# Optimization experiments

Measured on AMD Instinct MI355X. Metric: run time of the kernel, lower is better.

The kernel has to match this reference:

```python
import jax, jax.numpy as jnp
import numpy as np

NUM_FEATURES = 5
HIDDEN = 64
NUM_CLASSES = 5
N_NODES = 100000
N_EDGES = 1600000


def setup_inputs() -> dict:
    key = jax.random.key(0)
    ks = jax.random.split(key, 8)
    x = jax.random.normal(ks[0], (N_NODES, 4, NUM_FEATURES), dtype=jnp.float32)
    edge_index = jax.random.randint(ks[1], (2, N_EDGES), 0, N_NODES, dtype=jnp.int64)
    batch = jnp.zeros((N_NODES,), dtype=jnp.int64)
    # GCNConv layer 1: 5 -> 64, layer 2: 64 -> 64, output Linear: 64 -> 5
    W1 = jax.random.normal(ks[2], (NUM_FEATURES, HIDDEN), dtype=jnp.float32) / np.sqrt(NUM_FEATURES)
    b1 = jnp.zeros((HIDDEN,), dtype=jnp.float32)
    W2 = jax.random.normal(ks[3], (HIDDEN, HIDDEN), dtype=jnp.float32) / np.sqrt(HIDDEN)
    b2 = jnp.zeros((HIDDEN,), dtype=jnp.float32)
    Wout = jax.random.normal(ks[4], (HIDDEN, NUM_CLASSES), dtype=jnp.float32) / np.sqrt(HIDDEN)
    bout = jnp.zeros((NUM_CLASSES,), dtype=jnp.float32)
    return {"x": x, "edge_index": edge_index, "batch": batch,
            "W1": W1, "b1": b1, "W2": W2, "b2": b2, "Wout": Wout, "bout": bout}


def reference(x, edge_index, batch, W1, b1, W2, b2, Wout, bout):
    N = x.shape[0]
    src, dst = edge_index[0], edge_index[1]
    # GCN symmetric normalization with self-loops: deg counts incoming edges + self loop
    deg = jax.ops.segment_sum(jnp.ones(src.shape, jnp.float32), dst, num_segments=N) + 1.0
    dinv_sqrt = jax.lax.rsqrt(deg)
    norm = dinv_sqrt[src] * dinv_sqrt[dst]            # [E]
    self_norm = (1.0 / deg)[:, None]                  # self-loop weight deg^-1

    def gcn_conv(h, W, b):
        h = h @ W                                     # [N, out]
        agg = jax.ops.segment_sum(h[src] * norm[:, None], dst, num_segments=N)
        return agg + h * self_norm + b

    h = jax.nn.relu(gcn_conv(x[:, -1, :], W1, b1))    # [N, HIDDEN]
    h = jax.nn.relu(gcn_conv(h, W2, b2))              # [N, HIDDEN]
    return jax.nn.softmax(h @ Wout + bout, axis=1)    # [N, 5]
```

## Files before the change

kernel.cpp:

```cpp
#include <hip/hip_runtime.h>
#include <hip/hip_fp16.h>

#define HID 64
#define NF 5
#define NC 5

#define WSH 9
#define WINN 512
#define NBMAX 256
#define SRCB 17
#define NBLK 512


__global__ __launch_bounds__(512) void k_bcount(const int* __restrict__ dst, int E, int chunk,
                                                int nb, int* __restrict__ cntmat) {
    __shared__ int cnt[NBMAX];
    int t = threadIdx.x;
    for (int i = t; i < nb; i += 512) cnt[i] = 0;
    __syncthreads();
    int c0 = blockIdx.x * chunk;
    int c1 = c0 + chunk; if (c1 > E) c1 = E;
    for (int i = c0 + t * 4; i < c1; i += 512 * 4) {
        if (i + 3 < c1) {
            int4 d4 = *reinterpret_cast<const int4*>(dst + i);
            atomicAdd(&cnt[d4.x >> WSH], 1);
            atomicAdd(&cnt[d4.y >> WSH], 1);
            atomicAdd(&cnt[d4.z >> WSH], 1);
            atomicAdd(&cnt[d4.w >> WSH], 1);
        } else {
            for (int k = i; k < c1; ++k) atomicAdd(&cnt[dst[k] >> WSH], 1);
        }
    }
    __syncthreads();
    for (int i = t; i < nb; i += 512) cntmat[blockIdx.x * nb + i] = cnt[i];
}

__global__ __launch_bounds__(NBLK) void k_wscan(int* __restrict__ cntmat, int nb,
                                                int* __restrict__ btot) {
    __shared__ int s[NBLK];
    int b = blockIdx.x;
    int t = threadIdx.x;
    int v = cntmat[t * nb + b];
    s[t] = v;
    __syncthreads();
    for (int o = 1; o < NBLK; o <<= 1) {
        int u = (t >= o) ? s[t - o] : 0;
        __syncthreads();
        s[t] += u;
        __syncthreads();
    }
    cntmat[t * nb + b] = s[t] - v;
    if (t == NBLK - 1) btot[b] = s[t];
}

__global__ __launch_bounds__(256) void k_bscan2(const int* __restrict__ btot, int nb, int N,
                                                int* __restrict__ bbase,
                                                int* __restrict__ offsets) {
    __shared__ int s[256];
    int t = threadIdx.x;
    int v = (t < nb) ? btot[t] : 0;
    s[t] = v;
    __syncthreads();
    for (int o = 1; o < 256; o <<= 1) {
        int u = (t >= o) ? s[t - o] : 0;
        __syncthreads();
        s[t] += u;
        __syncthreads();
    }
    if (t < nb) bbase[t] = s[t] - v;
    if (t == nb - 1) { bbase[nb] = s[t]; offsets[N] = s[t]; }
}

__global__ __launch_bounds__(512) void k_bfill(const int* __restrict__ src,
                                               const int* __restrict__ dst, int E, int chunk,
                                               int nb, const int* __restrict__ bbase,
                                               const int* __restrict__ cntmat,
                                               unsigned int* __restrict__ pairbuf) {
    __shared__ int wcur[NBMAX];
    int t = threadIdx.x;
    int blk = blockIdx.x;
    for (int i = t; i < nb; i += 512)
        wcur[i] = bbase[i] + cntmat[blk * nb + i];
    __syncthreads();
    int c0 = blk * chunk;
    int c1 = c0 + chunk; if (c1 > E) c1 = E;
    for (int i = c0 + t * 4; i < c1; i += 512 * 4) {
        if (i + 3 < c1) {
            int4 d4 = *reinterpret_cast<const int4*>(dst + i);
            int4 s4 = *reinterpret_cast<const int4*>(src + i);
            int p;
            p = atomicAdd(&wcur[d4.x >> WSH], 1);
            pairbuf[p] = ((unsigned)(d4.x & (WINN - 1)) << SRCB) | (unsigned)s4.x;
            p = atomicAdd(&wcur[d4.y >> WSH], 1);
            pairbuf[p] = ((unsigned)(d4.y & (WINN - 1)) << SRCB) | (unsigned)s4.y;
            p = atomicAdd(&wcur[d4.z >> WSH], 1);
            pairbuf[p] = ((unsigned)(d4.z & (WINN - 1)) << SRCB) | (unsigned)s4.z;
            p = atomicAdd(&wcur[d4.w >> WSH], 1);
            pairbuf[p] = ((unsigned)(d4.w & (WINN - 1)) << SRCB) | (unsigned)s4.w;
        } else {
            for (int k = i; k < c1; ++k) {
                int d = dst[k];
                int p = atomicAdd(&wcur[d >> WSH], 1);
                pairbuf[p] = ((unsigned)(d & (WINN - 1)) << SRCB) | (unsigned)src[k];
            }
        }
    }
}

__global__ __launch_bounds__(WINN) void k_csr(const unsigned int* __restrict__ pairbuf,
                                              const int* __restrict__ bbase, int N,
                                              const float* __restrict__ x,
                                              int* __restrict__ offsets,
                                              int* __restrict__ csr_src,
                                              float* __restrict__ dinv,
                                              float* __restrict__ xs8) {
    int b = blockIdx.x, t = threadIdx.x;
    int lane = t & 63, w = t >> 6;
    int winStart = b << WSH;
    int rbeg = bbase[b], rend = bbase[b + 1];
    __shared__ int deg[WINN];
    __shared__ int cur[WINN];
    __shared__ int wsum[8];
    deg[t] = 0;
    __syncthreads();
    for (int p = rbeg + t; p < rend; p += WINN)
        atomicAdd(&deg[pairbuf[p] >> SRCB], 1);
    __syncthreads();
    int v = deg[t];
    int inc = v;
#pragma unroll
    for (int o = 1; o < 64; o <<= 1) {
        int u = __shfl_up(inc, o, 64);
        if (lane >= o) inc += u;
    }
    if (lane == 63) wsum[w] = inc;
    __syncthreads();
    int wbase = 0;
#pragma unroll
    for (int i = 0; i < 8; ++i) wbase += (i < w) ? wsum[i] : 0;
    int excl = wbase + inc - v;
    int node = winStart + t;
    if (node < N) {
        int base = rbeg + excl;
        offsets[node] = base;
        cur[t] = base;
        float dv = rsqrtf((float)v + 1.0f);
        dinv[node] = dv;
        const float* xr = x + (size_t)node * (4 * NF) + 3 * NF;
        float4 v0, v1;
        v0.x = xr[0] * dv; v0.y = xr[1] * dv; v0.z = xr[2] * dv; v0.w = xr[3] * dv;
        v1.x = xr[4] * dv; v1.y = 0.f; v1.z = 0.f; v1.w = 0.f;
        float4* xp = reinterpret_cast<float4*>(xs8 + (size_t)node * 8);
        xp[0] = v0;
        xp[1] = v1;
    }
    __syncthreads();
    for (int p = rbeg + t; p < rend; p += WINN) {
        unsigned u = pairbuf[p];
        int dl = u >> SRCB;
        int sn = u & ((1u << SRCB) - 1);
        int pos = atomicAdd(&cur[dl], 1);
        csr_src[pos] = sn;
    }
}


__global__ __launch_bounds__(256) void k_aggX(const float* __restrict__ xs8,
                                              const float* __restrict__ W1,
                                              const int* __restrict__ offsets,
                                              const int* __restrict__ csr_src,
                                              const float* __restrict__ dinv,
                                              const float* __restrict__ b1,
                                              __half* __restrict__ g1, int N) {
    int wid = (blockIdx.x * blockDim.x + threadIdx.x) >> 6;
    int lane = threadIdx.x & 63;
    int g = lane >> 1;
    int h = lane & 1;
    float w0 = W1[0 * HID + lane], w1 = W1[1 * HID + lane], w2 = W1[2 * HID + lane],
          w3 = W1[3 * HID + lane], w4 = W1[4 * HID + lane];
    if (wid >= N) return;
    int e0 = offsets[wid], e1 = offsets[wid + 1];
    float4 acc = {0.f, 0.f, 0.f, 0.f};
    int ee = e0 + g;
    int s = (ee < e1) ? csr_src[ee] : -1;
    for (int e = e0; e < e1; e += 32) {
        int cs = s;
        int en = e + 32 + g;
        s = (en < e1) ? csr_src[en] : -1;
        bool p = (cs >= 0);
        int csc = p ? cs : 0;
        float4 v = *reinterpret_cast<const float4*>(xs8 + (size_t)csc * 8 + (h << 2));
        if (p) { acc.x += v.x; acc.y += v.y; acc.z += v.z; acc.w += v.w; }
    }
    if (g == 0) {
        float4 v = *reinterpret_cast<const float4*>(xs8 + (size_t)wid * 8 + (h << 2));
        acc.x += v.x; acc.y += v.y; acc.z += v.z; acc.w += v.w;
    }
#pragma unroll
    for (int o = 2; o < 64; o <<= 1) {
        acc.x += __shfl_xor(acc.x, o, 64);
        acc.y += __shfl_xor(acc.y, o, 64);
        acc.z += __shfl_xor(acc.z, o, 64);
        acc.w += __shfl_xor(acc.w, o, 64);
    }
    float a0 = __shfl(acc.x, 0, 2), a1 = __shfl(acc.y, 0, 2),
          a2 = __shfl(acc.z, 0, 2), a3 = __shfl(acc.w, 0, 2),
          a4 = __shfl(acc.x, 1, 2);
    float dv = dinv[wid];
    float sres = a0 * w0 + a1 * w1 + a2 * w2 + a3 * w3 + a4 * w4;
    float r = fmaxf(fmaf(dv, sres, b1[lane]), 0.f) * dv;
    g1[(size_t)wid * HID + lane] = __float2half(r);
}

__global__ __launch_bounds__(256) void k_aggG(const __half* __restrict__ g1,
                                              const int* __restrict__ offsets,
                                              const int* __restrict__ csr_src,
                                              const float* __restrict__ dinv,
                                              __half* __restrict__ aggH, int N) {
    int wid = (blockIdx.x * blockDim.x + threadIdx.x) >> 6;
    if (wid >= N) return;
    int lane = threadIdx.x & 63;
    int g = lane >> 3;
    int f8 = (lane & 7) << 3;
    int e0 = offsets[wid], e1 = offsets[wid + 1];
    float acc[8];
#pragma unroll
    for (int i = 0; i < 8; ++i) acc[i] = 0.f;
    int ee = e0 + g;
    int s0 = (ee < e1) ? csr_src[ee] : -1;
    int s1 = (ee + 8 < e1) ? csr_src[ee + 8] : -1;
    int s2 = (ee + 16 < e1) ? csr_src[ee + 16] : -1;
    int s3 = (ee + 24 < e1) ? csr_src[ee + 24] : -1;
    for (int e = e0; e < e1; e += 32) {
        int cs0 = s0, cs1 = s1, cs2 = s2, cs3 = s3;
        int nb0 = e + 32 + g;
        s0 = (nb0 < e1) ? csr_src[nb0] : -1;
        s1 = (nb0 + 8 < e1) ? csr_src[nb0 + 8] : -1;
        s2 = (nb0 + 16 < e1) ? csr_src[nb0 + 16] : -1;
        s3 = (nb0 + 24 < e1) ? csr_src[nb0 + 24] : -1;
        bool p0 = (cs0 >= 0), p1 = (cs1 >= 0), p2 = (cs2 >= 0), p3 = (cs3 >= 0);
        int c0 = p0 ? cs0 : 0, c1 = p1 ? cs1 : 0, c2 = p2 ? cs2 : 0, c3 = p3 ? cs3 : 0;
        float4 raw0 = *reinterpret_cast<const float4*>(g1 + (size_t)c0 * HID + f8);
        float4 raw1 = *reinterpret_cast<const float4*>(g1 + (size_t)c1 * HID + f8);
        float4 raw2 = *reinterpret_cast<const float4*>(g1 + (size_t)c2 * HID + f8);
        float4 raw3 = *reinterpret_cast<const float4*>(g1 + (size_t)c3 * HID + f8);
        if (p0) {
            float2 q0 = __half22float2(*reinterpret_cast<__half2*>(&raw0.x));
            float2 q1 = __half22float2(*reinterpret_cast<__half2*>(&raw0.y));
            float2 q2 = __half22float2(*reinterpret_cast<__half2*>(&raw0.z));
            float2 q3 = __half22float2(*reinterpret_cast<__half2*>(&raw0.w));
            acc[0] += q0.x; acc[1] += q0.y; acc[2] += q1.x; acc[3] += q1.y;
            acc[4] += q2.x; acc[5] += q2.y; acc[6] += q3.x; acc[7] += q3.y;
        }
        if (p1) {
            float2 q0 = __half22float2(*reinterpret_cast<__half2*>(&raw1.x));
            float2 q1 = __half22float2(*reinterpret_cast<__half2*>(&raw1.y));
            float2 q2 = __half22float2(*reinterpret_cast<__half2*>(&raw1.z));
            float2 q3 = __half22float2(*reinterpret_cast<__half2*>(&raw1.w));
            acc[0] += q0.x; acc[1] += q0.y; acc[2] += q1.x; acc[3] += q1.y;
            acc[4] += q2.x; acc[5] += q2.y; acc[6] += q3.x; acc[7] += q3.y;
        }
        if (p2) {
            float2 q0 = __half22float2(*reinterpret_cast<__half2*>(&raw2.x));
            float2 q1 = __half22float2(*reinterpret_cast<__half2*>(&raw2.y));
            float2 q2 = __half22float2(*reinterpret_cast<__half2*>(&raw2.z));
            float2 q3 = __half22float2(*reinterpret_cast<__half2*>(&raw2.w));
            acc[0] += q0.x; acc[1] += q0.y; acc[2] += q1.x; acc[3] += q1.y;
            acc[4] += q2.x; acc[5] += q2.y; acc[6] += q3.x; acc[7] += q3.y;
        }
        if (p3) {
            float2 q0 = __half22float2(*reinterpret_cast<__half2*>(&raw3.x));
            float2 q1 = __half22float2(*reinterpret_cast<__half2*>(&raw3.y));
            float2 q2 = __half22float2(*reinterpret_cast<__half2*>(&raw3.z));
            float2 q3 = __half22float2(*reinterpret_cast<__half2*>(&raw3.w));
            acc[0] += q0.x; acc[1] += q0.y; acc[2] += q1.x; acc[3] += q1.y;
            acc[4] += q2.x; acc[5] += q2.y; acc[6] += q3.x; acc[7] += q3.y;
        }
    }
#pragma unroll
    for (int o = 8; o < 64; o <<= 1) {
#pragma unroll
        for (int i = 0; i < 8; ++i) acc[i] += __shfl_xor(acc[i], o, 64);
    }
    if (lane < 8) {
        float4 raw = *reinterpret_cast<const float4*>(g1 + (size_t)wid * HID + f8);
        float2 q0 = __half22float2(*reinterpret_cast<__half2*>(&raw.x));
        float2 q1 = __half22float2(*reinterpret_cast<__half2*>(&raw.y));
        float2 q2 = __half22float2(*reinterpret_cast<__half2*>(&raw.z));
        float2 q3 = __half22float2(*reinterpret_cast<__half2*>(&raw.w));
        float dv = dinv[wid];
        float4 st;
        *reinterpret_cast<__half2*>(&st.x) = __floats2half2_rn(dv * (acc[0] + q0.x), dv * (acc[1] + q0.y));
        *reinterpret_cast<__half2*>(&st.y) = __floats2half2_rn(dv * (acc[2] + q1.x), dv * (acc[3] + q1.y));
        *reinterpret_cast<__half2*>(&st.z) = __floats2half2_rn(dv * (acc[4] + q2.x), dv * (acc[5] + q2.y));
        *reinterpret_cast<__half2*>(&st.w) = __floats2half2_rn(dv * (acc[6] + q3.x), dv * (acc[7] + q3.y));
        *reinterpret_cast<float4*>(aggH + (size_t)wid * HID + f8) = st;
    }
}

__global__ __launch_bounds__(256) void k_fuse(const __half* __restrict__ aggH,
                                              const float* __restrict__ W2,
                                              const float* __restrict__ b2,
                                              const float* __restrict__ Wout,
                                              const float* __restrict__ bout,
                                              float* __restrict__ out, int N) {
    __shared__ float4 sh4[64][17];
    __shared__ float4 sW4[64 * 16];
    __shared__ float  swout[64][NC];
    __shared__ float  sb2[64];
    __shared__ float  sbout[8];
    int tx = threadIdx.x;
    int nb0 = blockIdx.x * 64;

    const float4* W2_4 = reinterpret_cast<const float4*>(W2);
    for (int i = tx; i < 64 * 16; i += 256) sW4[i] = W2_4[i];
    const float4* aggH4 = reinterpret_cast<const float4*>(aggH);
    for (int i = tx; i < 64 * 8; i += 256) {
        int row = i >> 3, h8 = i & 7;
        int node = nb0 + row;
        float4 raw = {0.f, 0.f, 0.f, 0.f};
        if (node < N) raw = aggH4[(size_t)node * 8 + h8];
        float2 q0 = __half22float2(*reinterpret_cast<__half2*>(&raw.x));
        float2 q1 = __half22float2(*reinterpret_cast<__half2*>(&raw.y));
        float2 q2 = __half22float2(*reinterpret_cast<__half2*>(&raw.z));
        float2 q3 = __half22float2(*reinterpret_cast<__half2*>(&raw.w));
        sh4[row][h8 * 2]     = make_float4(q0.x, q0.y, q1.x, q1.y);
        sh4[row][h8 * 2 + 1] = make_float4(q2.x, q2.y, q3.x, q3.y);
    }
    if (tx < 64) sb2[tx] = b2[tx];
    for (int i = tx; i < 64 * NC; i += 256) swout[i / NC][i % NC] = Wout[i];
    if (tx < NC) sbout[tx] = bout[tx];
    __syncthreads();

    int ty = tx >> 4;
    int txl = tx & 15;

    float acc[4][4];
#pragma unroll
    for (int j = 0; j < 4; ++j)
#pragma unroll
        for (int i = 0; i < 4; ++i) acc[j][i] = 0.f;

    for (int k4 = 0; k4 < 16; ++k4) {
        float4 w0 = sW4[(k4 * 4 + 0) * 16 + txl];
        float4 w1 = sW4[(k4 * 4 + 1) * 16 + txl];
        float4 w2 = sW4[(k4 * 4 + 2) * 16 + txl];
        float4 w3 = sW4[(k4 * 4 + 3) * 16 + txl];
#pragma unroll
        for (int j = 0; j < 4; ++j) {
            float4 hq = sh4[ty * 4 + j][k4];
            acc[j][0] = fmaf(hq.x, w0.x, fmaf(hq.y, w1.x, fmaf(hq.z, w2.x, fmaf(hq.w, w3.x, acc[j][0]))));
            acc[j][1] = fmaf(hq.x, w0.y, fmaf(hq.y, w1.y, fmaf(hq.z, w2.y, fmaf(hq.w, w3.y, acc[j][1]))));
            acc[j][2] = fmaf(hq.x, w0.z, fmaf(hq.y, w1.z, fmaf(hq.z, w2.z, fmaf(hq.w, w3.z, acc[j][2]))));
            acc[j][3] = fmaf(hq.x, w0.w, fmaf(hq.y, w1.w, fmaf(hq.z, w2.w, fmaf(hq.w, w3.w, acc[j][3]))));
        }
    }

    float pl[4][NC];
#pragma unroll
    for (int j = 0; j < 4; ++j)
#pragma unroll
        for (int c = 0; c < NC; ++c) pl[j][c] = 0.f;
#pragma unroll
    for (int j = 0; j < 4; ++j) {
#pragma unroll
        for (int i = 0; i < 4; ++i) {
            int f = txl * 4 + i;
            float h2 = fmaxf(acc[j][i] + sb2[f], 0.f);
#pragma unroll
            for (int c = 0; c < NC; ++c) pl[j][c] = fmaf(h2, swout[f][c], pl[j][c]);
        }
    }
#pragma unroll
    for (int o = 1; o < 16; o <<= 1) {
#pragma unroll
        for (int j = 0; j < 4; ++j)
#pragma unroll
            for (int c = 0; c < NC; ++c) pl[j][c] += __shfl_xor(pl[j][c], o, 64);
    }
    if (txl == 0) {
#pragma unroll
        for (int j = 0; j < 4; ++j) {
            int node = nb0 + ty * 4 + j;
            if (node < N) {
                float lg[NC];
#pragma unroll
                for (int c = 0; c < NC; ++c) lg[c] = pl[j][c] + sbout[c];
                float m = lg[0];
#pragma unroll
                for (int c = 1; c < NC; ++c) m = fmaxf(m, lg[c]);
                float ssum = 0.f, ex[NC];
#pragma unroll
                for (int c = 0; c < NC; ++c) { ex[c] = __expf(lg[c] - m); ssum += ex[c]; }
                float inv = 1.0f / ssum;
#pragma unroll
                for (int c = 0; c < NC; ++c) out[(size_t)node * NC + c] = ex[c] * inv;
            }
        }
    }
}


extern "C" void kernel_launch(void* const* d_in, const int* in_sizes, int n_in,
                              void* d_out, int out_size, void* d_ws, size_t ws_size,
                              hipStream_t stream) {
    const float* x   = (const float*)d_in[0];
    const int*   ei  = (const int*)d_in[1];
    const float* W1  = (const float*)d_in[3];
    const float* b1  = (const float*)d_in[4];
    const float* W2  = (const float*)d_in[5];
    const float* b2  = (const float*)d_in[6];
    const float* Wo  = (const float*)d_in[7];
    const float* bo  = (const float*)d_in[8];
    float* out = (float*)d_out;

    const int N = in_sizes[2];
    const int E = in_sizes[1] / 2;

    size_t off = 0;
    char* base = (char*)d_ws;
    auto alloc = [&](size_t bytes) -> void* {
        off = (off + 255) & ~(size_t)255;
        void* r = base + off;
        off += bytes;
        return r;
    };
    int*      cntmat  = (int*)alloc((size_t)NBLK * NBMAX * 4);
    int*      btot    = (int*)alloc((size_t)NBMAX * 4);
    int*      bbase   = (int*)alloc(((size_t)NBMAX + 1) * 4);
    unsigned* pairbuf = (unsigned*)alloc((size_t)E * 4);
    int*      offsets = (int*)alloc(((size_t)N + 1) * 4);
    int*      csr_src = (int*)alloc((size_t)E * 4);
    float*    dinv    = (float*)alloc((size_t)N * 4);
    float*    xs8     = (float*)alloc((size_t)N * 8 * 4);
    __half*   g1      = (__half*)alloc((size_t)N * HID * 2);
    __half*   aggH    = (__half*)alloc((size_t)N * HID * 2);

    const int T = 256;
    int gNF = ((N * HID) + T - 1) / T;

    const int* src = ei;
    const int* dst = ei + E;

    int nb = (N + WINN - 1) >> WSH;
    int chunk = (((E + NBLK - 1) / NBLK) + 3) & ~3;

    k_bcount<<<NBLK, 512, 0, stream>>>(dst, E, chunk, nb, cntmat);
    k_wscan<<<nb, NBLK, 0, stream>>>(cntmat, nb, btot);
    k_bscan2<<<1, 256, 0, stream>>>(btot, nb, N, bbase, offsets);
    k_bfill<<<NBLK, 512, 0, stream>>>(src, dst, E, chunk, nb, bbase, cntmat, pairbuf);
    k_csr<<<nb, WINN, 0, stream>>>(pairbuf, bbase, N, x, offsets, csr_src, dinv, xs8);

    k_aggX<<<gNF, T, 0, stream>>>(xs8, W1, offsets, csr_src, dinv, b1, g1, N);

    k_aggG<<<gNF, T, 0, stream>>>(g1, offsets, csr_src, dinv, aggH, N);

    int nbF = (N + 63) / 64;
    k_fuse<<<nbF, 256, 0, stream>>>(aggH, W2, b2, Wo, bo, out, N);
}
```

Before: 203.4 us.

## Fuse second GCN aggregation with W2 matmul, output linear and softmax

Merges the layer-2 neighbor aggregation kernel and the dense W2/Wout/softmax kernel into one kernel. Each wave handles 8 nodes, computes the aggregated row, then does the 64x64 matvec via shuffles against W2 in shared memory. This drops the fp16 aggH intermediate and its global round trip, at the cost of loading W2 into LDS per block and a less efficient per-node matvec. It also halves NBLK for the CSR build kernels.

```diff
diff --git a/kernel.cpp b/kernel.cpp
--- a/kernel.cpp
+++ b/kernel.cpp
@@ -9,7 +9,7 @@
 #define WINN 512
 #define NBMAX 256
 #define SRCB 17
-#define NBLK 512
+#define NBLK 256
 
 
 __global__ __launch_bounds__(512) void k_bcount(const int* __restrict__ dst, int E, int chunk,
@@ -212,190 +212,136 @@
     g1[(size_t)wid * HID + lane] = __float2half(r);
 }
 
-__global__ __launch_bounds__(256) void k_aggG(const __half* __restrict__ g1,
+__global__ __launch_bounds__(256) void k_aggF(const __half* __restrict__ g1,
                                               const int* __restrict__ offsets,
                                               const int* __restrict__ csr_src,
                                               const float* __restrict__ dinv,
-                                              __half* __restrict__ aggH, int N) {
-    int wid = (blockIdx.x * blockDim.x + threadIdx.x) >> 6;
-    if (wid >= N) return;
-    int lane = threadIdx.x & 63;
+                                              const float* __restrict__ W2,
+                                              const float* __restrict__ b2,
+                                              const float* __restrict__ Wout,
+                                              const float* __restrict__ bout,
+                                              float* __restrict__ out, int N) {
+    __shared__ float sW2[HID * HID];
+    __shared__ float swout[HID * NC];
+    __shared__ float sb2[HID];
+    __shared__ float sbout[8];
+    int tx = threadIdx.x;
+    const float4* W2_4 = reinterpret_cast<const float4*>(W2);
+    float4* sW2_4 = reinterpret_cast<float4*>(sW2);
+    for (int i = tx; i < HID * 16; i += 256) sW2_4[i] = W2_4[i];
+    for (int i = tx; i < HID * NC; i += 256) swout[i] = Wout[i];
+    if (tx < HID) sb2[tx] = b2[tx];
+    if (tx < NC) sbout[tx] = bout[tx];
+    __syncthreads();
+
+    int w = tx >> 6, lane = tx & 63;
     int g = lane >> 3;
     int f8 = (lane & 7) << 3;
-    int e0 = offsets[wid], e1 = offsets[wid + 1];
-    float acc[8];
-#pragma unroll
-    for (int i = 0; i < 8; ++i) acc[i] = 0.f;
-    int ee = e0 + g;
-    int s0 = (ee < e1) ? csr_src[ee] : -1;
-    int s1 = (ee + 8 < e1) ? csr_src[ee + 8] : -1;
-    int s2 = (ee + 16 < e1) ? csr_src[ee + 16] : -1;
-    int s3 = (ee + 24 < e1) ? csr_src[ee + 24] : -1;
-    for (int e = e0; e < e1; e += 32) {
-        int cs0 = s0, cs1 = s1, cs2 = s2, cs3 = s3;
-        int nb0 = e + 32 + g;
-        s0 = (nb0 < e1) ? csr_src[nb0] : -1;
-        s1 = (nb0 + 8 < e1) ? csr_src[nb0 + 8] : -1;
-        s2 = (nb0 + 16 < e1) ? csr_src[nb0 + 16] : -1;
-        s3 = (nb0 + 24 < e1) ? csr_src[nb0 + 24] : -1;
-        bool p0 = (cs0 >= 0), p1 = (cs1 >= 0), p2 = (cs2 >= 0), p3 = (cs3 >= 0);
-        int c0 = p0 ? cs0 : 0, c1 = p1 ? cs1 : 0, c2 = p2 ? cs2 : 0, c3 = p3 ? cs3 : 0;
-        float4 raw0 = *reinterpret_cast<const float4*>(g1 + (size_t)c0 * HID + f8);
-        float4 raw1 = *reinterpret_cast<const float4*>(g1 + (size_t)c1 * HID + f8);
-        float4 raw2 = *reinterpret_cast<const float4*>(g1 + (size_t)c2 * HID + f8);
-        float4 raw3 = *reinterpret_cast<const float4*>(g1 + (size_t)c3 * HID + f8);
-        if (p0) {
-            float2 q0 = __half22float2(*reinterpret_cast<__half2*>(&raw0.x));
-            float2 q1 = __half22float2(*reinterpret_cast<__half2*>(&raw0.y));
-            float2 q2 = __half22float2(*reinterpret_cast<__half2*>(&raw0.z));
-            float2 q3 = __half22float2(*reinterpret_cast<__half2*>(&raw0.w));
-            acc[0] += q0.x; acc[1] += q0.y; acc[2] += q1.x; acc[3] += q1.y;
-            acc[4] += q2.x; acc[5] += q2.y; acc[6] += q3.x; acc[7] += q3.y;
-        }
-        if (p1) {
-            float2 q0 = __half22float2(*reinterpret_cast<__half2*>(&raw1.x));
-            float2 q1 = __half22float2(*reinterpret_cast<__half2*>(&raw1.y));
-            float2 q2 = __half22float2(*reinterpret_cast<__half2*>(&raw1.z));
-            float2 q3 = __half22float2(*reinterpret_cast<__half2*>(&raw1.w));
-            acc[0] += q0.x; acc[1] += q0.y; acc[2] += q1.x; acc[3] += q1.y;
-            acc[4] += q2.x; acc[5] += q2.y; acc[6] += q3.x; acc[7] += q3.y;
-        }
-        if (p2) {
-            float2 q0 = __half22float2(*reinterpret_cast<__half2*>(&raw2.x));
-            float2 q1 = __half22float2(*reinterpret_cast<__half2*>(&raw2.y));
-            float2 q2 = __half22float2(*reinterpret_cast<__half2*>(&raw2.z));
-            float2 q3 = __half22float2(*reinterpret_cast<__half2*>(&raw2.w));
-            acc[0] += q0.x; acc[1] += q0.y; acc[2] += q1.x; acc[3] += q1.y;
-            acc[4] += q2.x; acc[5] += q2.y; acc[6] += q3.x; acc[7] += q3.y;
-        }
-        if (p3) {
-            float2 q0 = __half22float2(*reinterpret_cast<__half2*>(&raw3.x));
-            float2 q1 = __half22float2(*reinterpret_cast<__half2*>(&raw3.y));
-            float2 q2 = __half22float2(*reinterpret_cast<__half2*>(&raw3.z));
-            float2 q3 = __half22float2(*reinterpret_cast<__half2*>(&raw3.w));
-            acc[0] += q0.x; acc[1] += q0.y; acc[2] += q1.x; acc[3] += q1.y;
-            acc[4] += q2.x; acc[5] += q2.y; acc[6] += q3.x; acc[7] += q3.y;
-        }
-    }
-#pragma unroll
-    for (int o = 8; o < 64; o <<= 1) {
-#pragma unroll
-        for (int i = 0; i < 8; ++i) acc[i] += __shfl_xor(acc[i], o, 64);
-    }
-    if (lane < 8) {
+    int nodeBase = blockIdx.x * 32 + w * 8;
+
+    for (int j = 0; j < 8; ++j) {
+        int wid = nodeBase + j;
+        if (wid >= N) break;
+        int e0 = offsets[wid], e1 = offsets[wid + 1];
+        float acc[8];
+#pragma unroll
+        for (int i = 0; i < 8; ++i) acc[i] = 0.f;
+        int ee = e0 + g;
+        int s0 = (ee < e1) ? csr_src[ee] : -1;
+        int s1 = (ee + 8 < e1) ? csr_src[ee + 8] : -1;
+        int s2 = (ee + 16 < e1) ? csr_src[ee + 16] : -1;
+        int s3 = (ee + 24 < e1) ? csr_src[ee + 24] : -1;
+        for (int e = e0; e < e1; e += 32) {
+            int cs0 = s0, cs1 = s1, cs2 = s2, cs3 = s3;
+            int nx = e + 32 + g;
+            s0 = (nx < e1) ? csr_src[nx] : -1;
+            s1 = (nx + 8 < e1) ? csr_src[nx + 8] : -1;
+            s2 = (nx + 16 < e1) ? csr_src[nx + 16] : -1;
+            s3 = (nx + 24 < e1) ? csr_src[nx + 24] : -1;
+            bool p0 = (cs0 >= 0), p1 = (cs1 >= 0), p2 = (cs2 >= 0), p3 = (cs3 >= 0);
+            int c0 = p0 ? cs0 : 0, c1 = p1 ? cs1 : 0, c2 = p2 ? cs2 : 0, c3 = p3 ? cs3 : 0;
+            float4 raw0 = *reinterpret_cast<const float4*>(g1 + (size_t)c0 * HID + f8);
+            float4 raw1 = *reinterpret_cast<const float4*>(g1 + (size_t)c1 * HID + f8);
+            float4 raw2 = *reinterpret_cast<const float4*>(g1 + (size_t)c2 * HID + f8);
+            float4 raw3 = *reinterpret_cast<const float4*>(g1 + (size_t)c3 * HID + f8);
+            if (p0) {
+                float2 q0 = __half22float2(*reinterpret_cast<__half2*>(&raw0.x));
+                float2 q1 = __half22float2(*reinterpret_cast<__half2*>(&raw0.y));
+                float2 q2 = __half22float2(*reinterpret_cast<__half2*>(&raw0.z));
+                float2 q3 = __half22float2(*reinterpret_cast<__half2*>(&raw0.w));
+                acc[0] += q0.x; acc[1] += q0.y; acc[2] += q1.x; acc[3] += q1.y;
+                acc[4] += q2.x; acc[5] += q2.y; acc[6] += q3.x; acc[7] += q3.y;
+            }
+            if (p1) {
+                float2 q0 = __half22float2(*reinterpret_cast<__half2*>(&raw1.x));
+                float2 q1 = __half22float2(*reinterpret_cast<__half2*>(&raw1.y));
+                float2 q2 = __half22float2(*reinterpret_cast<__half2*>(&raw1.z));
+                float2 q3 = __half22float2(*reinterpret_cast<__half2*>(&raw1.w));
+                acc[0] += q0.x; acc[1] += q0.y; acc[2] += q1.x; acc[3] += q1.y;
+                acc[4] += q2.x; acc[5] += q2.y; acc[6] += q3.x; acc[7] += q3.y;
+            }
+            if (p2) {
+                float2 q0 = __half22float2(*reinterpret_cast<__half2*>(&raw2.x));
+                float2 q1 = __half22float2(*reinterpret_cast<__half2*>(&raw2.y));
+                float2 q2 = __half22float2(*reinterpret_cast<__half2*>(&raw2.z));
+                float2 q3 = __half22float2(*reinterpret_cast<__half2*>(&raw2.w));
+                acc[0] += q0.x; acc[1] += q0.y; acc[2] += q1.x; acc[3] += q1.y;
+                acc[4] += q2.x; acc[5] += q2.y; acc[6] += q3.x; acc[7] += q3.y;
+            }
+            if (p3) {
+                float2 q0 = __half22float2(*reinterpret_cast<__half2*>(&raw3.x));
+                float2 q1 = __half22float2(*reinterpret_cast<__half2*>(&raw3.y));
+                float2 q2 = __half22float2(*reinterpret_cast<__half2*>(&raw3.z));
+                float2 q3 = __half22float2(*reinterpret_cast<__half2*>(&raw3.w));
+                acc[0] += q0.x; acc[1] += q0.y; acc[2] += q1.x; acc[3] += q1.y;
+                acc[4] += q2.x; acc[5] += q2.y; acc[6] += q3.x; acc[7] += q3.y;
+            }
+        }
+#pragma unroll
+        for (int o = 8; o < 64; o <<= 1) {
+#pragma unroll
+            for (int i = 0; i < 8; ++i) acc[i] += __shfl_xor(acc[i], o, 64);
+        }
         float4 raw = *reinterpret_cast<const float4*>(g1 + (size_t)wid * HID + f8);
         float2 q0 = __half22float2(*reinterpret_cast<__half2*>(&raw.x));
         float2 q1 = __half22float2(*reinterpret_cast<__half2*>(&raw.y));
         float2 q2 = __half22float2(*reinterpret_cast<__half2*>(&raw.z));
         float2 q3 = __half22float2(*reinterpret_cast<__half2*>(&raw.w));
         float dv = dinv[wid];
-        float4 st;
-        *reinterpret_cast<__half2*>(&st.x) = __floats2half2_rn(dv * (acc[0] + q0.x), dv * (acc[1] + q0.y));
-        *reinterpret_cast<__half2*>(&st.y) = __floats2half2_rn(dv * (acc[2] + q1.x), dv * (acc[3] + q1.y));
-        *reinterpret_cast<__half2*>(&st.z) = __floats2half2_rn(dv * (acc[4] + q2.x), dv * (acc[5] + q2.y));
-        *reinterpret_cast<__half2*>(&st.w) = __floats2half2_rn(dv * (acc[6] + q3.x), dv * (acc[7] + q3.y));
-        *reinterpret_cast<float4*>(aggH + (size_t)wid * HID + f8) = st;
-    }
-}
-
-__global__ __launch_bounds__(256) void k_fuse(const __half* __restrict__ aggH,
-                                              const float* __restrict__ W2,
-                                              const float* __restrict__ b2,
-                                              const float* __restrict__ Wout,
-                                              const float* __restrict__ bout,
-                                              float* __restrict__ out, int N) {
-    __shared__ float4 sh4[64][17];
-    __shared__ float4 sW4[64 * 16];
-    __shared__ float  swout[64][NC];
-    __shared__ float  sb2[64];
-    __shared__ float  sbout[8];
-    int tx = threadIdx.x;
-    int nb0 = blockIdx.x * 64;
-
-    const float4* W2_4 = reinterpret_cast<const float4*>(W2);
-    for (int i = tx; i < 64 * 16; i += 256) sW4[i] = W2_4[i];
-    const float4* aggH4 = reinterpret_cast<const float4*>(aggH);
-    for (int i = tx; i < 64 * 8; i += 256) {
-        int row = i >> 3, h8 = i & 7;
-        int node = nb0 + row;
-        float4 raw = {0.f, 0.f, 0.f, 0.f};
-        if (node < N) raw = aggH4[(size_t)node * 8 + h8];
-        float2 q0 = __half22float2(*reinterpret_cast<__half2*>(&raw.x));
-        float2 q1 = __half22float2(*reinterpret_cast<__half2*>(&raw.y));
-        float2 q2 = __half22float2(*reinterpret_cast<__half2*>(&raw.z));
-        float2 q3 = __half22float2(*reinterpret_cast<__half2*>(&raw.w));
-        sh4[row][h8 * 2]     = make_float4(q0.x, q0.y, q1.x, q1.y);
-        sh4[row][h8 * 2 + 1] = make_float4(q2.x, q2.y, q3.x, q3.y);
-    }
-    if (tx < 64) sb2[tx] = b2[tx];
-    for (int i = tx; i < 64 * NC; i += 256) swout[i / NC][i % NC] = Wout[i];
-    if (tx < NC) sbout[tx] = bout[tx];
-    __syncthreads();
-
-    int ty = tx >> 4;
-    int txl = tx & 15;
-
-    float acc[4][4];
-#pragma unroll
-    for (int j = 0; j < 4; ++j)
-#pragma unroll
-        for (int i = 0; i < 4; ++i) acc[j][i] = 0.f;
-
-    for (int k4 = 0; k4 < 16; ++k4) {
-        float4 w0 = sW4[(k4 * 4 + 0) * 16 + txl];
-        float4 w1 = sW4[(k4 * 4 + 1) * 16 + txl];
-        float4 w2 = sW4[(k4 * 4 + 2) * 16 + txl];
-        float4 w3 = sW4[(k4 * 4 + 3) * 16 + txl];
-#pragma unroll
-        for (int j = 0; j < 4; ++j) {
-            float4 hq = sh4[ty * 4 + j][k4];
-            acc[j][0] = fmaf(hq.x, w0.x, fmaf(hq.y, w1.x, fmaf(hq.z, w2.x, fmaf(hq.w, w3.x, acc[j][0]))));
-            acc[j][1] = fmaf(hq.x, w0.y, fmaf(hq.y, w1.y, fmaf(hq.z, w2.y, fmaf(hq.w, w3.y, acc[j][1]))));
-            acc[j][2] = fmaf(hq.x, w0.z, fmaf(hq.y, w1.z, fmaf(hq.z, w2.z, fmaf(hq.w, w3.z, acc[j][2]))));
-            acc[j][3] = fmaf(hq.x, w0.w, fmaf(hq.y, w1.w, fmaf(hq.z, w2.w, fmaf(hq.w, w3.w, acc[j][3]))));
-        }
-    }
-
-    float pl[4][NC];
-#pragma unroll
-    for (int j = 0; j < 4; ++j)
-#pragma unroll
-        for (int c = 0; c < NC; ++c) pl[j][c] = 0.f;
-#pragma unroll
-    for (int j = 0; j < 4; ++j) {
-#pragma unroll
-        for (int i = 0; i < 4; ++i) {
-            int f = txl * 4 + i;
-            float h2 = fmaxf(acc[j][i] + sb2[f], 0.f);
-#pragma unroll
-            for (int c = 0; c < NC; ++c) pl[j][c] = fmaf(h2, swout[f][c], pl[j][c]);
-        }
-    }
-#pragma unroll
-    for (int o = 1; o < 16; o <<= 1) {
-#pragma unroll
-        for (int j = 0; j < 4; ++j)
-#pragma unroll
-            for (int c = 0; c < NC; ++c) pl[j][c] += __shfl_xor(pl[j][c], o, 64);
-    }
-    if (txl == 0) {
-#pragma unroll
-        for (int j = 0; j < 4; ++j) {
-            int node = nb0 + ty * 4 + j;
-            if (node < N) {
-                float lg[NC];
-#pragma unroll
-                for (int c = 0; c < NC; ++c) lg[c] = pl[j][c] + sbout[c];
-                float m = lg[0];
-#pragma unroll
-                for (int c = 1; c < NC; ++c) m = fmaxf(m, lg[c]);
-                float ssum = 0.f, ex[NC];
-#pragma unroll
-                for (int c = 0; c < NC; ++c) { ex[c] = __expf(lg[c] - m); ssum += ex[c]; }
-                float inv = 1.0f / ssum;
-#pragma unroll
-                for (int c = 0; c < NC; ++c) out[(size_t)node * NC + c] = ex[c] * inv;
-            }
+        float row[8];
+        row[0] = dv * (acc[0] + q0.x); row[1] = dv * (acc[1] + q0.y);
+        row[2] = dv * (acc[2] + q1.x); row[3] = dv * (acc[3] + q1.y);
+        row[4] = dv * (acc[4] + q2.x); row[5] = dv * (acc[5] + q2.y);
+        row[6] = dv * (acc[6] + q3.x); row[7] = dv * (acc[7] + q3.y);
+        float h2 = sb2[lane];
+#pragma unroll
+        for (int c = 0; c < 8; ++c) {
+#pragma unroll
+            for (int i = 0; i < 8; ++i) {
+                float rk = __shfl(row[i], c, 8);
+                h2 = fmaf(rk, sW2[(c * 8 + i) * HID + lane], h2);
+            }
+        }
+        h2 = fmaxf(h2, 0.f);
+        float pl[NC];
+#pragma unroll
+        for (int c = 0; c < NC; ++c) pl[c] = h2 * swout[lane * NC + c];
+#pragma unroll
+        for (int o = 1; o < 64; o <<= 1) {
+#pragma unroll
+            for (int c = 0; c < NC; ++c) pl[c] += __shfl_xor(pl[c], o, 64);
+        }
+        if (lane < NC) {
+            float lg[NC];
+#pragma unroll
+            for (int c = 0; c < NC; ++c) lg[c] = pl[c] + sbout[c];
+            float m = lg[0];
+#pragma unroll
+            for (int c = 1; c < NC; ++c) m = fmaxf(m, lg[c]);
+            float ssum = 0.f, ex[NC];
+#pragma unroll
+            for (int c = 0; c < NC; ++c) { ex[c] = __expf(lg[c] - m); ssum += ex[c]; }
+            out[(size_t)wid * NC + lane] = ex[lane] / ssum;
         }
     }
 }
@@ -434,7 +380,6 @@
     float*    dinv    = (float*)alloc((size_t)N * 4);
     float*    xs8     = (float*)alloc((size_t)N * 8 * 4);
     __half*   g1      = (__half*)alloc((size_t)N * HID * 2);
-    __half*   aggH    = (__half*)alloc((size_t)N * HID * 2);
 
     const int T = 256;
     int gNF = ((N * HID) + T - 1) / T;
@@ -453,8 +398,6 @@
 
     k_aggX<<<gNF, T, 0, stream>>>(xs8, W1, offsets, csr_src, dinv, b1, g1, N);
 
-    k_aggG<<<gNF, T, 0, stream>>>(g1, offsets, csr_src, dinv, aggH, N);
-
-    int nbF = (N + 63) / 64;
-    k_fuse<<<nbF, 256, 0, stream>>>(aggH, W2, b2, Wo, bo, out, N);
-}
+    int gF = (N + 31) / 32;
+    k_aggF<<<gF, 256, 0, stream>>>(g1, offsets, csr_src, dinv, W2, b2, Wo, bo, out, N);
+}
```

Result: slower. 304.0 us (+49.4%).
